# Performance work log

Measured on AMD Instinct MI355X. Metric: run time of the kernel, lower is better.

The kernel has to match this reference:

```python
import jax, jax.numpy as jnp
import numpy as np

N_NODES = 100000
N_EDGES = 1600000
N_GRAPHS = 256
D = 32  # node/edge/global feature dim


def setup_inputs() -> dict:
    key = jax.random.key(0)
    k1, k2, k3, k4, k5, k6 = jax.random.split(key, 6)
    x = jax.random.normal(k1, (N_NODES, D), dtype=jnp.float32)
    edge_index = jax.random.randint(k2, (2, N_EDGES), 0, N_NODES, dtype=jnp.int64)
    edge_attr = jax.random.normal(k3, (N_EDGES, D), dtype=jnp.float32)
    u = jax.random.normal(k4, (N_GRAPHS, D), dtype=jnp.float32)
    batch = jnp.sort(jax.random.randint(k5, (N_NODES,), 0, N_GRAPHS, dtype=jnp.int64))
    W = jax.random.normal(k6, (3 * D, D), dtype=jnp.float32) * (1.0 / np.sqrt(3 * D))
    b = jnp.zeros((D,), dtype=jnp.float32)
    return {"x": x, "edge_index": edge_index, "edge_attr": edge_attr,
            "u": u, "batch": batch, "W": W, "b": b}


def reference(x, edge_index, edge_attr, u, batch, W, b):
    src = edge_index[0]
    num_graphs = u.shape[0]
    # scatter-sum node features by graph id
    node_agg = jax.ops.segment_sum(x, batch, num_segments=num_graphs)
    # scatter-sum edge features by graph id of their source node
    edge_agg = jax.ops.segment_sum(edge_attr, batch[src], num_segments=num_graphs)
    global_input = jnp.concatenate([node_agg, edge_agg, u], axis=-1)  # [B, 3D]
    return jax.nn.relu(global_input @ W + b)
```

## Files before the change

kernel.cpp:

```cpp
#include <hip/hip_runtime.h>

#define N_NODES   100000
#define N_EDGES   1600000
#define N_GRAPHS  256
#define D         32
#define GD        (N_GRAPHS * D)
#define LSTRIDE   257
#define NBLK      256
#define SCALE_F   1048576.0f
#define INV_SCALE 9.5367431640625e-07f

typedef float f32x4 __attribute__((ext_vector_type(4)));

__global__ __launch_bounds__(1024) void edge_stream_kernel(
        const float* __restrict__ ea,
        const int* __restrict__ src,
        const int* __restrict__ batch,
        int* __restrict__ epart ) {
    __shared__ int lds[D * LSTRIDE];
    for (int i = threadIdx.x; i < D * LSTRIDE; i += 1024) lds[i] = 0;
    __syncthreads();

    const f32x4* __restrict__ ea4 = (const f32x4*)ea;
    const int total = N_EDGES * (D / 4);
    const int S     = NBLK * 1024;
    const int S2    = 2 * S;
    const int i0    = blockIdx.x * 1024 + threadIdx.x;
    const int NIT   = (total + S2 - 1) / S2;
    const int cbase = ((i0 & 7) * 4) * LSTRIDE;

    int iA = i0, iB = i0 + S;
    f32x4 v0, v1;
    int g0, g1, s0n, s1n;
    {
        const int sA = src[min(iA, total - 1) >> 3];
        const int sB = src[min(iB, total - 1) >> 3];
        g0 = batch[sA];
        g1 = batch[sB];
        const f32x4 t0 = ea4[min(iA, total - 1)];
        const f32x4 t1 = ea4[min(iB, total - 1)];
        v0 = t0 * ((iA < total) ? 1.f : 0.f);
        v1 = t1 * ((iB < total) ? 1.f : 0.f);
        s0n = src[min(iA + S2, total - 1) >> 3];
        s1n = src[min(iB + S2, total - 1) >> 3];
    }

    for (int k = 0; k < NIT; ++k) {
        const int iA2 = iA + S2, iB2 = iB + S2;
        const int s0nn = src[min(iA2 + S2, total - 1) >> 3];
        const int s1nn = src[min(iB2 + S2, total - 1) >> 3];
        const int g0n = batch[s0n];
        const int g1n = batch[s1n];
        const f32x4 t0 = ea4[min(iA2, total - 1)];
        const f32x4 t1 = ea4[min(iB2, total - 1)];
        const f32x4 v0n = t0 * ((iA2 < total) ? 1.f : 0.f);
        const f32x4 v1n = t1 * ((iB2 < total) ? 1.f : 0.f);

        const int b0 = cbase + g0;
        atomicAdd(&lds[b0              ], __float2int_rn(v0.x * SCALE_F));
        atomicAdd(&lds[b0 +     LSTRIDE], __float2int_rn(v0.y * SCALE_F));
        atomicAdd(&lds[b0 + 2 * LSTRIDE], __float2int_rn(v0.z * SCALE_F));
        atomicAdd(&lds[b0 + 3 * LSTRIDE], __float2int_rn(v0.w * SCALE_F));
        const int b1 = cbase + g1;
        atomicAdd(&lds[b1              ], __float2int_rn(v1.x * SCALE_F));
        atomicAdd(&lds[b1 +     LSTRIDE], __float2int_rn(v1.y * SCALE_F));
        atomicAdd(&lds[b1 + 2 * LSTRIDE], __float2int_rn(v1.z * SCALE_F));
        atomicAdd(&lds[b1 + 3 * LSTRIDE], __float2int_rn(v1.w * SCALE_F));

        iA = iA2; iB = iB2;
        v0 = v0n; v1 = v1n; g0 = g0n; g1 = g1n; s0n = s0nn; s1n = s1nn;
    }
    __syncthreads();

    int* __restrict__ my = epart + (size_t)blockIdx.x * GD;
    for (int j = threadIdx.x; j < GD; j += 1024)
        my[j] = lds[(j & 31) * LSTRIDE + (j >> 5)];
}

__global__ __launch_bounds__(1024) void finish_kernel(
        const float* __restrict__ x,
        const int* __restrict__ batch,
        const int* __restrict__ epart,
        const float* __restrict__ u,
        const float* __restrict__ W,
        const float* __restrict__ bias,
        float* __restrict__ out) {
    const int g = blockIdx.x;
    __shared__ float  Ws[3 * D * D];
    __shared__ float4 red[1024];
    __shared__ int4   ered[128][9];
    __shared__ float  accN[D], accE[D], ush[D];

    for (int j = threadIdx.x; j < 3 * D * D; j += 1024) Ws[j] = W[j];
    if (threadIdx.x < D) ush[threadIdx.x] = u[g * D + threadIdx.x];

    int lo = 0, hi = N_NODES;
    while (lo < hi) { const int m = (lo + hi) >> 1; if (batch[m] < g) lo = m + 1; else hi = m; }
    const int r0 = lo;
    hi = N_NODES;
    while (lo < hi) { const int m = (lo + hi) >> 1; if (batch[m] < g + 1) lo = m + 1; else hi = m; }
    const int r1 = lo;

    {
        const int s = threadIdx.x >> 3;
        const int c = threadIdx.x & 7;
        const float4* __restrict__ x4 = (const float4*)x;
        float4 a = make_float4(0.f, 0.f, 0.f, 0.f);
        for (int r = r0 + s; r < r1; r += 128) {
            const float4 v = x4[r * 8 + c];
            a.x += v.x; a.y += v.y; a.z += v.z; a.w += v.w;
        }
        red[threadIdx.x] = a;
    }

    {
        const int pg = threadIdx.x >> 3;
        const int q  = threadIdx.x & 7;
        const int4* __restrict__ ep4 = (const int4*)epart + (size_t)g * 8 + q;
        int4 s4 = ep4[(size_t)pg * (GD / 4)];
        const int4 t4 = ep4[(size_t)(pg + 128) * (GD / 4)];
        s4.x += t4.x; s4.y += t4.y; s4.z += t4.z; s4.w += t4.w;
        ered[pg][q] = s4;
    }
    __syncthreads();

    if (threadIdx.x < 256) {
        float4 t = red[threadIdx.x];
        const float4 b1 = red[threadIdx.x + 256];
        const float4 b2 = red[threadIdx.x + 512];
        const float4 b3 = red[threadIdx.x + 768];
        t.x += b1.x + b2.x + b3.x; t.y += b1.y + b2.y + b3.y;
        t.z += b1.z + b2.z + b3.z; t.w += b1.w + b2.w + b3.w;
        red[threadIdx.x] = t;
    } else if (threadIdx.x < 512) {
        const int t2 = threadIdx.x - 256;
        const int j = t2 >> 3, q = t2 & 7;
        int4 s4 = ered[j][q];
        const int4 a1 = ered[j + 32][q];
        const int4 a2 = ered[j + 64][q];
        const int4 a3 = ered[j + 96][q];
        s4.x += a1.x + a2.x + a3.x; s4.y += a1.y + a2.y + a3.y;
        s4.z += a1.z + a2.z + a3.z; s4.w += a1.w + a2.w + a3.w;
        ered[j][q] = s4;
    }
    __syncthreads();

    if (threadIdx.x < 8) {
        float4 t = make_float4(0.f, 0.f, 0.f, 0.f);
        #pragma unroll
        for (int s2 = 0; s2 < 32; ++s2) {
            const float4 b = red[s2 * 8 + threadIdx.x];
            t.x += b.x; t.y += b.y; t.z += b.z; t.w += b.w;
        }
        ((float4*)accN)[threadIdx.x] = t;
    } else if (threadIdx.x < 16) {
        const int q = threadIdx.x - 8;
        int4 s4 = make_int4(0, 0, 0, 0);
        #pragma unroll
        for (int j = 0; j < 32; ++j) {
            const int4 b = ered[j][q];
            s4.x += b.x; s4.y += b.y; s4.z += b.z; s4.w += b.w;
        }
        accE[q * 4 + 0] = (float)s4.x * INV_SCALE;
        accE[q * 4 + 1] = (float)s4.y * INV_SCALE;
        accE[q * 4 + 2] = (float)s4.z * INV_SCALE;
        accE[q * 4 + 3] = (float)s4.w * INV_SCALE;
    }
    __syncthreads();

    if (threadIdx.x < D) {
        const int d = threadIdx.x;
        float sacc = bias[d];
        #pragma unroll
        for (int kk = 0; kk < D; ++kk) sacc += accN[kk] * Ws[kk * D + d];
        #pragma unroll
        for (int kk = 0; kk < D; ++kk) sacc += accE[kk] * Ws[(D + kk) * D + d];
        #pragma unroll
        for (int kk = 0; kk < D; ++kk) sacc += ush[kk] * Ws[(2 * D + kk) * D + d];
        out[g * D + d] = fmaxf(sacc, 0.f);
    }
}

extern "C" void kernel_launch(void* const* d_in, const int* in_sizes, int n_in,
                              void* d_out, int out_size, void* d_ws, size_t ws_size,
                              hipStream_t stream) {
    const float* x     = (const float*)d_in[0];
    const int*   ei    = (const int*)  d_in[1];
    const float* ea    = (const float*)d_in[2];
    const float* u     = (const float*)d_in[3];
    const int*   batch = (const int*)  d_in[4];
    const float* W     = (const float*)d_in[5];
    const float* bias  = (const float*)d_in[6];
    float*       out   = (float*)d_out;

    int* epart = (int*)d_ws;

    edge_stream_kernel<<<NBLK, 1024, 0, stream>>>(ea, ei, batch, epart);
    finish_kernel     <<<N_GRAPHS, 1024, 0, stream>>>(x, batch, epart, u, W, bias, out);
}
```

Baseline: 46.77 us.

## Move per-graph node reduction into edge kernel as extra blocks

Adds 256 extra blocks to the edge streaming kernel. Each one does the binary search and the node-feature segment sum for one graph and writes partial results to workspace. The finish kernel then only reads the precomputed node sums, reduces the edge partials and applies the matmul. The intent is to overlap the node reduction with the bandwidth-bound edge pass and shorten the finish kernel's critical path. In exchange, node blocks may compete with edge blocks for CUs and bandwidth, and the grid is larger.

```diff
diff --git a/kernel.cpp b/kernel.cpp
--- a/kernel.cpp
+++ b/kernel.cpp
@@ -12,12 +12,58 @@
 
 typedef float f32x4 __attribute__((ext_vector_type(4)));
 
-__global__ __launch_bounds__(1024) void edge_stream_kernel(
+__global__ __launch_bounds__(1024) void edge_node_kernel(
         const float* __restrict__ ea,
         const int* __restrict__ src,
         const int* __restrict__ batch,
-        int* __restrict__ epart ) {
+        const float* __restrict__ x,
+        int* __restrict__ epart ,
+        float* __restrict__ npart ) {
     __shared__ int lds[D * LSTRIDE];
+
+    if (blockIdx.x >= NBLK) {
+        const int g = blockIdx.x - NBLK;
+        float4* red = (float4*)lds;
+        int lo = 0, hi = N_NODES;
+        while (lo < hi) { const int m = (lo + hi) >> 1; if (batch[m] < g) lo = m + 1; else hi = m; }
+        const int r0 = lo;
+        hi = N_NODES;
+        while (lo < hi) { const int m = (lo + hi) >> 1; if (batch[m] < g + 1) lo = m + 1; else hi = m; }
+        const int r1 = lo;
+
+        const int s = threadIdx.x >> 3;
+        const int c = threadIdx.x & 7;
+        const float4* __restrict__ x4 = (const float4*)x;
+
+        float4 a = make_float4(0.f, 0.f, 0.f, 0.f);
+        for (int r = r0 + s; r < r1; r += 128) {
+            const float4 v = x4[r * 8 + c];
+            a.x += v.x; a.y += v.y; a.z += v.z; a.w += v.w;
+        }
+        red[threadIdx.x] = a;
+        __syncthreads();
+        if (threadIdx.x < 256) {
+            float4 t = red[threadIdx.x];
+            const float4 b1 = red[threadIdx.x + 256];
+            const float4 b2 = red[threadIdx.x + 512];
+            const float4 b3 = red[threadIdx.x + 768];
+            t.x += b1.x + b2.x + b3.x; t.y += b1.y + b2.y + b3.y;
+            t.z += b1.z + b2.z + b3.z; t.w += b1.w + b2.w + b3.w;
+            red[threadIdx.x] = t;
+        }
+        __syncthreads();
+        if (threadIdx.x < 8) {
+            float4 t = make_float4(0.f, 0.f, 0.f, 0.f);
+            #pragma unroll
+            for (int s2 = 0; s2 < 32; ++s2) {
+                const float4 b = red[s2 * 8 + threadIdx.x];
+                t.x += b.x; t.y += b.y; t.z += b.z; t.w += b.w;
+            }
+            ((float4*)(npart + (size_t)g * D))[threadIdx.x] = t;
+        }
+        return;
+    }
+
     for (int i = threadIdx.x; i < D * LSTRIDE; i += 1024) lds[i] = 0;
     __syncthreads();
 
@@ -78,39 +124,21 @@
 }
 
 __global__ __launch_bounds__(1024) void finish_kernel(
-        const float* __restrict__ x,
-        const int* __restrict__ batch,
+        const float* __restrict__ npart,
         const int* __restrict__ epart,
         const float* __restrict__ u,
         const float* __restrict__ W,
         const float* __restrict__ bias,
         float* __restrict__ out) {
     const int g = blockIdx.x;
-    __shared__ float  Ws[3 * D * D];
-    __shared__ float4 red[1024];
-    __shared__ int4   ered[128][9];
-    __shared__ float  accN[D], accE[D], ush[D];
+    __shared__ float Ws[3 * D * D];
+    __shared__ int4  ered[128][9];
+    __shared__ float accN[D], accE[D], ush[D];
 
     for (int j = threadIdx.x; j < 3 * D * D; j += 1024) Ws[j] = W[j];
-    if (threadIdx.x < D) ush[threadIdx.x] = u[g * D + threadIdx.x];
-
-    int lo = 0, hi = N_NODES;
-    while (lo < hi) { const int m = (lo + hi) >> 1; if (batch[m] < g) lo = m + 1; else hi = m; }
-    const int r0 = lo;
-    hi = N_NODES;
-    while (lo < hi) { const int m = (lo + hi) >> 1; if (batch[m] < g + 1) lo = m + 1; else hi = m; }
-    const int r1 = lo;
-
-    {
-        const int s = threadIdx.x >> 3;
-        const int c = threadIdx.x & 7;
-        const float4* __restrict__ x4 = (const float4*)x;
-        float4 a = make_float4(0.f, 0.f, 0.f, 0.f);
-        for (int r = r0 + s; r < r1; r += 128) {
-            const float4 v = x4[r * 8 + c];
-            a.x += v.x; a.y += v.y; a.z += v.z; a.w += v.w;
-        }
-        red[threadIdx.x] = a;
+    if (threadIdx.x < D) {
+        ush [threadIdx.x] = u[g * D + threadIdx.x];
+        accN[threadIdx.x] = npart[g * D + threadIdx.x];
     }
 
     {
@@ -125,16 +153,7 @@
     __syncthreads();
 
     if (threadIdx.x < 256) {
-        float4 t = red[threadIdx.x];
-        const float4 b1 = red[threadIdx.x + 256];
-        const float4 b2 = red[threadIdx.x + 512];
-        const float4 b3 = red[threadIdx.x + 768];
-        t.x += b1.x + b2.x + b3.x; t.y += b1.y + b2.y + b3.y;
-        t.z += b1.z + b2.z + b3.z; t.w += b1.w + b2.w + b3.w;
-        red[threadIdx.x] = t;
-    } else if (threadIdx.x < 512) {
-        const int t2 = threadIdx.x - 256;
-        const int j = t2 >> 3, q = t2 & 7;
+        const int j = threadIdx.x >> 3, q = threadIdx.x & 7;
         int4 s4 = ered[j][q];
         const int4 a1 = ered[j + 32][q];
         const int4 a2 = ered[j + 64][q];
@@ -146,15 +165,7 @@
     __syncthreads();
 
     if (threadIdx.x < 8) {
-        float4 t = make_float4(0.f, 0.f, 0.f, 0.f);
-        #pragma unroll
-        for (int s2 = 0; s2 < 32; ++s2) {
-            const float4 b = red[s2 * 8 + threadIdx.x];
-            t.x += b.x; t.y += b.y; t.z += b.z; t.w += b.w;
-        }
-        ((float4*)accN)[threadIdx.x] = t;
-    } else if (threadIdx.x < 16) {
-        const int q = threadIdx.x - 8;
+        const int q = threadIdx.x;
         int4 s4 = make_int4(0, 0, 0, 0);
         #pragma unroll
         for (int j = 0; j < 32; ++j) {
@@ -193,8 +204,9 @@
     const float* bias  = (const float*)d_in[6];
     float*       out   = (float*)d_out;
 
-    int* epart = (int*)d_ws;
-
-    edge_stream_kernel<<<NBLK, 1024, 0, stream>>>(ea, ei, batch, epart);
-    finish_kernel     <<<N_GRAPHS, 1024, 0, stream>>>(x, batch, epart, u, W, bias, out);
+    float* npart = (float*)d_ws;
+    int*   epart = (int*)(npart + GD);
+
+    edge_node_kernel<<<NBLK + N_GRAPHS, 1024, 0, stream>>>(ea, ei, batch, x, epart, npart);
+    finish_kernel   <<<N_GRAPHS, 1024, 0, stream>>>(npart, epart, u, W, bias, out);
 }
```

Result: faster. 43.60 us (-6.8%).
